# Kernel optimization log

Measured on AMD Instinct MI355X. Metric: run time of the kernel, lower is better.

Reference implementation:

```python
import jax, jax.numpy as jnp
import numpy as np

BS, SLEN, EM = 32, 4096, 256


def setup_inputs() -> dict:
    key = jax.random.key(0)
    ks = jax.random.split(key, 8)
    word_embedded = jax.random.normal(ks[0], (BS, SLEN, EM), dtype=jnp.float32)
    # valid-token mask: first `length` tokens valid per row (True = keep)
    lengths = jax.random.randint(ks[1], (BS, 1), SLEN // 2, SLEN + 1)
    mask = jnp.arange(SLEN)[None, :] < lengths  # (BS, SLEN) bool
    s = 1.0 / np.sqrt(EM)
    w_query = jax.random.uniform(ks[2], (EM, 1), minval=-1.0, maxval=1.0, dtype=jnp.float32)  # Linear(1, em, bias=False)
    wq = jax.random.uniform(ks[3], (EM, EM), minval=-s, maxval=s, dtype=jnp.float32)
    bq = jax.random.uniform(ks[4], (EM,), minval=-s, maxval=s, dtype=jnp.float32)
    wk = jax.random.uniform(ks[5], (EM, EM), minval=-s, maxval=s, dtype=jnp.float32)
    bk = jax.random.uniform(ks[6], (EM,), minval=-s, maxval=s, dtype=jnp.float32)
    se = 1.0 / np.sqrt(2 * EM)
    we = jax.random.uniform(ks[7], (1, 2 * EM), minval=-se, maxval=se, dtype=jnp.float32)
    be = jnp.zeros((1,), dtype=jnp.float32)
    return {"word_embedded": word_embedded, "mask": mask, "w_query": w_query,
            "wq": wq, "bq": bq, "wk": wk, "bk": bk, "we": we, "be": be}


def reference(word_embedded, mask, w_query, wq, bq, wk, bk, we, be):
    bs, slen, em = word_embedded.shape
    # query = Linear(1, em, no bias) applied to ones -> each row is w_query[:, 0]
    q = jnp.broadcast_to(w_query[:, 0], (bs, em))          # (bs, em)
    qp = jax.nn.relu(q @ wq.T + bq)                        # (bs, em); dropout is identity at eval
    k = jax.nn.relu(word_embedded @ wk.T + bk)             # (bs, slen, em)
    # proj_e(tanh(cat(q, k))) == tanh(q)@we_q + tanh(k)@we_k + be (tanh is elementwise),
    # so we avoid materializing the (bs, slen, 2*em) concat.
    we_q, we_k = we[0, :em], we[0, em:]
    energy = jnp.tanh(qp) @ we_q                           # (bs,)
    energy = energy[:, None] + jnp.tanh(k) @ we_k + be[0]  # (bs, slen)
    # torch: energy.masked_fill_(~mask, 1e-45)
    energy = jnp.where(mask, energy, jnp.float32(1e-45))
    attn_weights = jax.nn.softmax(energy, axis=1)          # (bs, slen)
    sent_embedded = jnp.einsum('bs,bse->be', attn_weights, word_embedded)  # (bs, em)
    return sent_embedded
```

## Files before the change

### kernel.cpp

```cpp
#include <hip/hip_runtime.h>

#define BS   32
#define SLEN 4096
#define EM   256
#define NROWS (BS * SLEN)

typedef __attribute__((ext_vector_type(8))) short bf16x8;
typedef __attribute__((ext_vector_type(4))) float f32x4;

#define WS_WKB   0
#define WS_EN    32768
#define WS_CONST 163840
#define WS_W     163856
#define WS_PART  294928

__device__ inline short f2bf(float x) {
  union { float f; unsigned u; } v; v.f = x;
  unsigned r = v.u + 0x7fffu + ((v.u >> 16) & 1u);
  return (short)(r >> 16);
}

#define GLOAD_LDS16(g, l)                                                  \
  __builtin_amdgcn_global_load_lds(                                        \
      (const __attribute__((address_space(1))) unsigned int*)(g),          \
      (__attribute__((address_space(3))) unsigned int*)(l), 16, 0, 0)

__global__ __launch_bounds__(256) void k0_cvt(const float* __restrict__ wk,
                                              unsigned short* __restrict__ wkb) {
  int idx = (blockIdx.x * 256 + threadIdx.x) * 4;
  float4 v = *(const float4*)(wk + idx);
  ushort4 o;
  o.x = (unsigned short)f2bf(v.x);
  o.y = (unsigned short)f2bf(v.y);
  o.z = (unsigned short)f2bf(v.z);
  o.w = (unsigned short)f2bf(v.w);
  *(ushort4*)(wkb + idx) = o;
}

__global__ __launch_bounds__(256) void k0b_qscalar(const float* __restrict__ w_query,
                                                   const float* __restrict__ wq,
                                                   const float* __restrict__ bq,
                                                   const float* __restrict__ we,
                                                   const float* __restrict__ be,
                                                   float* __restrict__ outc) {
  int t = threadIdx.x;
  float a = 0.f;
  const float* row = wq + (size_t)t * EM;
#pragma unroll 8
  for (int j = 0; j < EM; ++j) a = fmaf(row[j], w_query[j], a);
  a += bq[t];
  float v = we[t] * tanhf(fmaxf(a, 0.f));
#pragma unroll
  for (int off = 32; off >= 1; off >>= 1) v += __shfl_xor(v, off, 64);
  __shared__ float red[4];
  if ((t & 63) == 0) red[t >> 6] = v;
  __syncthreads();
  if (t == 0) outc[0] = red[0] + red[1] + red[2] + red[3] + be[0];
}

__global__ __launch_bounds__(256) void k1_energy(const float* __restrict__ X,
                                                 const unsigned short* __restrict__ wkb,
                                                 const float* __restrict__ bk,
                                                 const float* __restrict__ we,
                                                 float* __restrict__ energy) {
  __shared__ char lds[40960];
  char* As = lds;
  char* Bs = lds + 8192;
  const int tid = threadIdx.x;
  const int l = tid & 63;
  const int wid = tid >> 6;
  const int wr = wid >> 1, wc = wid & 1;
  const int row0 = blockIdx.x * 64;

  f32x4 acc[2][8];
#pragma unroll
  for (int i = 0; i < 2; ++i)
#pragma unroll
    for (int n = 0; n < 8; ++n) acc[i][n] = (f32x4){0.f, 0.f, 0.f, 0.f};

  const int egl = l >> 3;
  const int cg = (l & 7) ^ egl;

  for (int it = 0; it < 4; ++it) {
    const int k0 = it * 64;
#pragma unroll
    for (int q = 0; q < 8; ++q) {
      int seg = wid * 8 + q;
      int e = seg * 8 + egl;
      const char* g = (const char*)wkb + (size_t)e * 512 + k0 * 2 + cg * 16;
      GLOAD_LDS16(g, Bs + seg * 1024);
    }
#pragma unroll
    for (int p = 0; p < 2; ++p) {
      int n = tid + p * 256;
      int r = n >> 3, c = n & 7;
      const float* src = X + (size_t)(row0 + r) * EM + k0 + c * 8;
      float4 v0 = *(const float4*)(src);
      float4 v1 = *(const float4*)(src + 4);
      bf16x8 pk;
      pk[0] = f2bf(v0.x); pk[1] = f2bf(v0.y); pk[2] = f2bf(v0.z); pk[3] = f2bf(v0.w);
      pk[4] = f2bf(v1.x); pk[5] = f2bf(v1.y); pk[6] = f2bf(v1.z); pk[7] = f2bf(v1.w);
      *(bf16x8*)(As + r * 128 + ((c ^ (r & 7)) * 16)) = pk;
    }
    __syncthreads();
#pragma unroll
    for (int s = 0; s < 2; ++s) {
      const int swz0 = ((s * 4 + (l >> 4)) ^ (l & 7)) * 16;
      bf16x8 af[2], bfr[8];
#pragma unroll
      for (int i = 0; i < 2; ++i) {
        int row = wr * 32 + i * 16 + (l & 15);
        af[i] = *(const bf16x8*)(As + row * 128 + swz0);
      }
#pragma unroll
      for (int n = 0; n < 8; ++n) {
        int e = wc * 128 + n * 16 + (l & 15);
        bfr[n] = *(const bf16x8*)(Bs + e * 128 + swz0);
      }
#pragma unroll
      for (int i = 0; i < 2; ++i)
#pragma unroll
        for (int n = 0; n < 8; ++n)
          acc[i][n] = __builtin_amdgcn_mfma_f32_16x16x32_bf16(af[i], bfr[n], acc[i][n], 0, 0, 0);
    }
    __syncthreads();
  }

  float bkv[8], wev[8];
#pragma unroll
  for (int n = 0; n < 8; ++n) {
    int e = wc * 128 + n * 16 + (l & 15);
    bkv[n] = bk[e];
    wev[n] = we[EM + e];
  }
  float* ep = (float*)lds;
#pragma unroll
  for (int i = 0; i < 2; ++i) {
#pragma unroll
    for (int r = 0; r < 4; ++r) {
      float p = 0.f;
#pragma unroll
      for (int n = 0; n < 8; ++n) {
        float kv = fmaxf(acc[i][n][r] + bkv[n], 0.f);
        p += wev[n] * tanhf(kv);
      }
#pragma unroll
      for (int off = 1; off <= 8; off <<= 1) p += __shfl_xor(p, off, 64);
      if ((l & 15) == 0) {
        int row_local = wr * 32 + i * 16 + (l >> 4) * 4 + r;
        ep[row_local * 2 + wc] = p;
      }
    }
  }
  __syncthreads();
  if (tid < 64) energy[row0 + tid] = ep[tid * 2] + ep[tid * 2 + 1];
}

__global__ __launch_bounds__(256) void k2_softmax(const float* __restrict__ energy,
                                                  const unsigned char* __restrict__ mask,
                                                  const float* __restrict__ cptr,
                                                  float* __restrict__ wout) {
  const int b = blockIdx.x;
  const int t = threadIdx.x;
  const float C = cptr[0];
  const bool mask_is_byte = (mask[1] | mask[2] | mask[3]) != 0;
  const int* mask32 = (const int*)mask;
  const float* eb = energy + (size_t)b * SLEN;
  float v[16];
  float m = -3.4e38f;
#pragma unroll
  for (int i = 0; i < 16; ++i) {
    int s = t + i * 256;
    int mv = mask_is_byte ? (int)mask[(size_t)b * SLEN + s]
                          : mask32[(size_t)b * SLEN + s];
    float x = mv ? (eb[s] + C) : 1.4012984643248171e-45f;
    v[i] = x;
    m = fmaxf(m, x);
  }
  __shared__ float red[8];
#pragma unroll
  for (int off = 32; off >= 1; off >>= 1) m = fmaxf(m, __shfl_xor(m, off, 64));
  if ((t & 63) == 0) red[t >> 6] = m;
  __syncthreads();
  m = fmaxf(fmaxf(red[0], red[1]), fmaxf(red[2], red[3]));
  float s_ = 0.f;
#pragma unroll
  for (int i = 0; i < 16; ++i) {
    v[i] = expf(v[i] - m);
    s_ += v[i];
  }
#pragma unroll
  for (int off = 32; off >= 1; off >>= 1) s_ += __shfl_xor(s_, off, 64);
  if ((t & 63) == 0) red[4 + (t >> 6)] = s_;
  __syncthreads();
  float inv = 1.f / (red[4] + red[5] + red[6] + red[7]);
  float* wb = wout + (size_t)b * SLEN;
#pragma unroll
  for (int i = 0; i < 16; ++i) wb[t + i * 256] = v[i] * inv;
}

__global__ __launch_bounds__(256) void k3_wsum(const float* __restrict__ X,
                                               const float* __restrict__ w,
                                               float* __restrict__ part) {
  const int b = blockIdx.x >> 4;
  const int ch = blockIdx.x & 15;
  const int g = threadIdx.x >> 6;
  const int l = threadIdx.x & 63;
  const int s0 = ch * 256 + g * 64;
  const float* xb = X + (size_t)b * SLEN * EM;
  const float* wb = w + (size_t)b * SLEN;
  float4 acc = make_float4(0.f, 0.f, 0.f, 0.f);
#pragma unroll 4
  for (int i = 0; i < 64; ++i) {
    int s = s0 + i;
    float ws_ = wb[s];
    float4 v = *(const float4*)(xb + (size_t)s * EM + l * 4);
    acc.x = fmaf(ws_, v.x, acc.x);
    acc.y = fmaf(ws_, v.y, acc.y);
    acc.z = fmaf(ws_, v.z, acc.z);
    acc.w = fmaf(ws_, v.w, acc.w);
  }
  *(float4*)(part + ((size_t)((b * 16 + ch) * 4 + g)) * EM + l * 4) = acc;
}

__global__ __launch_bounds__(256) void k4_reduce(const float* __restrict__ part,
                                                 float* __restrict__ out) {
  const int b = blockIdx.x;
  const int e = threadIdx.x;
  float s = 0.f;
#pragma unroll 8
  for (int k = 0; k < 64; ++k) s += part[((size_t)b * 64 + k) * EM + e];
  out[(size_t)b * EM + e] = s;
}

extern "C" void kernel_launch(void* const* d_in, const int* in_sizes, int n_in,
                              void* d_out, int out_size, void* d_ws, size_t ws_size,
                              hipStream_t stream) {
  const float* X = (const float*)d_in[0];
  const unsigned char* mask = (const unsigned char*)d_in[1];
  const float* w_query = (const float*)d_in[2];
  const float* wq = (const float*)d_in[3];
  const float* bq = (const float*)d_in[4];
  const float* wk = (const float*)d_in[5];
  const float* bk = (const float*)d_in[6];
  const float* we = (const float*)d_in[7];
  const float* be = (const float*)d_in[8];
  float* out = (float*)d_out;
  float* ws = (float*)d_ws;

  unsigned short* wkb = (unsigned short*)(ws + WS_WKB);
  float* energy = ws + WS_EN;
  float* cscalar = ws + WS_CONST;
  float* weights = ws + WS_W;
  float* part = ws + WS_PART;

  k0_cvt<<<64, 256, 0, stream>>>(wk, wkb);
  k0b_qscalar<<<1, 256, 0, stream>>>(w_query, wq, bq, we, be, cscalar);
  k1_energy<<<NROWS / 64, 256, 0, stream>>>(X, wkb, bk, we, energy);
  k2_softmax<<<BS, 256, 0, stream>>>(energy, mask, cscalar, weights);
  k3_wsum<<<BS * 16, 256, 0, stream>>>(X, weights, part);
  k4_reduce<<<BS, 256, 0, stream>>>(part, out);
}
```

Before: 292.1 us.

## Load GEMM operands directly to registers, use fast tanh/exp, rebalance weighted-sum grid

The energy GEMM no longer stages X and Wk tiles through LDS with barriers. Each wave now loads its A fragments straight from global memory, converting to bf16 in registers, and reads B fragments directly from the bf16 weight buffer. tanhf and expf are replaced with fast exp-based approximations. The weighted-sum kernel uses twice as many blocks and reduces its four waves in LDS, which halves the partial buffer the final reduce reads. The trade-off is less data reuse across waves, since each wave re-reads Wk from cache, plus slightly lower accuracy from the approximate transcendentals.

```diff
diff --git a/kernel.cpp b/kernel.cpp
--- a/kernel.cpp
+++ b/kernel.cpp
@@ -20,10 +20,10 @@
   return (short)(r >> 16);
 }
 
-#define GLOAD_LDS16(g, l)                                                  \
-  __builtin_amdgcn_global_load_lds(                                        \
-      (const __attribute__((address_space(1))) unsigned int*)(g),          \
-      (__attribute__((address_space(3))) unsigned int*)(l), 16, 0, 0)
+__device__ inline float tanh_pos(float x) {
+  float e2 = __expf(2.f * x);
+  return 1.f - __fdividef(2.f, e2 + 1.f);
+}
 
 __global__ __launch_bounds__(256) void k0_cvt(const float* __restrict__ wk,
                                               unsigned short* __restrict__ wkb) {
@@ -49,7 +49,7 @@
 #pragma unroll 8
   for (int j = 0; j < EM; ++j) a = fmaf(row[j], w_query[j], a);
   a += bq[t];
-  float v = we[t] * tanhf(fmaxf(a, 0.f));
+  float v = we[t] * tanh_pos(fmaxf(a, 0.f));
 #pragma unroll
   for (int off = 32; off >= 1; off >>= 1) v += __shfl_xor(v, off, 64);
   __shared__ float red[4];
@@ -63,14 +63,15 @@
                                                  const float* __restrict__ bk,
                                                  const float* __restrict__ we,
                                                  float* __restrict__ energy) {
-  __shared__ char lds[40960];
-  char* As = lds;
-  char* Bs = lds + 8192;
+  __shared__ float ep[64][2];
   const int tid = threadIdx.x;
   const int l = tid & 63;
   const int wid = tid >> 6;
   const int wr = wid >> 1, wc = wid & 1;
+  const int lr = l & 15, lk = l >> 4;
   const int row0 = blockIdx.x * 64;
+  const float* xw = X + (size_t)(row0 + wr * 32 + lr) * EM;
+  const unsigned short* bw = wkb + (size_t)(wc * 128 + lr) * EM;
 
   f32x4 acc[2][8];
 #pragma unroll
@@ -78,62 +79,38 @@
 #pragma unroll
     for (int n = 0; n < 8; ++n) acc[i][n] = (f32x4){0.f, 0.f, 0.f, 0.f};
 
-  const int egl = l >> 3;
-  const int cg = (l & 7) ^ egl;
-
-  for (int it = 0; it < 4; ++it) {
-    const int k0 = it * 64;
-#pragma unroll
-    for (int q = 0; q < 8; ++q) {
-      int seg = wid * 8 + q;
-      int e = seg * 8 + egl;
-      const char* g = (const char*)wkb + (size_t)e * 512 + k0 * 2 + cg * 16;
-      GLOAD_LDS16(g, Bs + seg * 1024);
+#pragma unroll
+  for (int s = 0; s < 8; ++s) {
+    const int kf = s * 32 + lk * 8;
+    bf16x8 af[2];
+#pragma unroll
+    for (int i = 0; i < 2; ++i) {
+      const float* src = xw + (size_t)(i * 16) * EM + kf;
+      float4 v0 = *(const float4*)src;
+      float4 v1 = *(const float4*)(src + 4);
+      bf16x8 t;
+      t[0] = f2bf(v0.x); t[1] = f2bf(v0.y); t[2] = f2bf(v0.z); t[3] = f2bf(v0.w);
+      t[4] = f2bf(v1.x); t[5] = f2bf(v1.y); t[6] = f2bf(v1.z); t[7] = f2bf(v1.w);
+      af[i] = t;
     }
-#pragma unroll
-    for (int p = 0; p < 2; ++p) {
-      int n = tid + p * 256;
-      int r = n >> 3, c = n & 7;
-      const float* src = X + (size_t)(row0 + r) * EM + k0 + c * 8;
-      float4 v0 = *(const float4*)(src);
-      float4 v1 = *(const float4*)(src + 4);
-      bf16x8 pk;
-      pk[0] = f2bf(v0.x); pk[1] = f2bf(v0.y); pk[2] = f2bf(v0.z); pk[3] = f2bf(v0.w);
-      pk[4] = f2bf(v1.x); pk[5] = f2bf(v1.y); pk[6] = f2bf(v1.z); pk[7] = f2bf(v1.w);
-      *(bf16x8*)(As + r * 128 + ((c ^ (r & 7)) * 16)) = pk;
-    }
-    __syncthreads();
-#pragma unroll
-    for (int s = 0; s < 2; ++s) {
-      const int swz0 = ((s * 4 + (l >> 4)) ^ (l & 7)) * 16;
-      bf16x8 af[2], bfr[8];
-#pragma unroll
-      for (int i = 0; i < 2; ++i) {
-        int row = wr * 32 + i * 16 + (l & 15);
-        af[i] = *(const bf16x8*)(As + row * 128 + swz0);
-      }
-#pragma unroll
-      for (int n = 0; n < 8; ++n) {
-        int e = wc * 128 + n * 16 + (l & 15);
-        bfr[n] = *(const bf16x8*)(Bs + e * 128 + swz0);
-      }
-#pragma unroll
-      for (int i = 0; i < 2; ++i)
-#pragma unroll
-        for (int n = 0; n < 8; ++n)
-          acc[i][n] = __builtin_amdgcn_mfma_f32_16x16x32_bf16(af[i], bfr[n], acc[i][n], 0, 0, 0);
-    }
-    __syncthreads();
+    bf16x8 bfr[8];
+#pragma unroll
+    for (int n = 0; n < 8; ++n)
+      bfr[n] = *(const bf16x8*)(bw + (size_t)(n * 16) * EM + kf);
+#pragma unroll
+    for (int i = 0; i < 2; ++i)
+#pragma unroll
+      for (int n = 0; n < 8; ++n)
+        acc[i][n] = __builtin_amdgcn_mfma_f32_16x16x32_bf16(af[i], bfr[n], acc[i][n], 0, 0, 0);
   }
 
   float bkv[8], wev[8];
 #pragma unroll
   for (int n = 0; n < 8; ++n) {
-    int e = wc * 128 + n * 16 + (l & 15);
+    int e = wc * 128 + n * 16 + lr;
     bkv[n] = bk[e];
     wev[n] = we[EM + e];
   }
-  float* ep = (float*)lds;
 #pragma unroll
   for (int i = 0; i < 2; ++i) {
 #pragma unroll
@@ -142,18 +119,15 @@
 #pragma unroll
       for (int n = 0; n < 8; ++n) {
         float kv = fmaxf(acc[i][n][r] + bkv[n], 0.f);
-        p += wev[n] * tanhf(kv);
+        p += wev[n] * tanh_pos(kv);
       }
 #pragma unroll
       for (int off = 1; off <= 8; off <<= 1) p += __shfl_xor(p, off, 64);
-      if ((l & 15) == 0) {
-        int row_local = wr * 32 + i * 16 + (l >> 4) * 4 + r;
-        ep[row_local * 2 + wc] = p;
-      }
+      if (lr == 0) ep[wr * 32 + i * 16 + lk * 4 + r][wc] = p;
     }
   }
   __syncthreads();
-  if (tid < 64) energy[row0 + tid] = ep[tid * 2] + ep[tid * 2 + 1];
+  if (tid < 64) energy[row0 + tid] = ep[tid][0] + ep[tid][1];
 }
 
 __global__ __launch_bounds__(256) void k2_softmax(const float* __restrict__ energy,
@@ -186,7 +160,7 @@
   float s_ = 0.f;
 #pragma unroll
   for (int i = 0; i < 16; ++i) {
-    v[i] = expf(v[i] - m);
+    v[i] = __expf(v[i] - m);
     s_ += v[i];
   }
 #pragma unroll
@@ -202,16 +176,17 @@
 __global__ __launch_bounds__(256) void k3_wsum(const float* __restrict__ X,
                                                const float* __restrict__ w,
                                                float* __restrict__ part) {
-  const int b = blockIdx.x >> 4;
-  const int ch = blockIdx.x & 15;
+  __shared__ float red[4][EM];
+  const int b = blockIdx.x >> 5;
+  const int ch = blockIdx.x & 31;
   const int g = threadIdx.x >> 6;
   const int l = threadIdx.x & 63;
-  const int s0 = ch * 256 + g * 64;
+  const int s0 = ch * 128 + g * 32;
   const float* xb = X + (size_t)b * SLEN * EM;
   const float* wb = w + (size_t)b * SLEN;
   float4 acc = make_float4(0.f, 0.f, 0.f, 0.f);
 #pragma unroll 4
-  for (int i = 0; i < 64; ++i) {
+  for (int i = 0; i < 32; ++i) {
     int s = s0 + i;
     float ws_ = wb[s];
     float4 v = *(const float4*)(xb + (size_t)s * EM + l * 4);
@@ -220,7 +195,20 @@
     acc.z = fmaf(ws_, v.z, acc.z);
     acc.w = fmaf(ws_, v.w, acc.w);
   }
-  *(float4*)(part + ((size_t)((b * 16 + ch) * 4 + g)) * EM + l * 4) = acc;
+  *(float4*)(&red[g][l * 4]) = acc;
+  __syncthreads();
+  if (g == 0) {
+    float4 r0 = *(const float4*)(&red[0][l * 4]);
+    float4 r1 = *(const float4*)(&red[1][l * 4]);
+    float4 r2 = *(const float4*)(&red[2][l * 4]);
+    float4 r3 = *(const float4*)(&red[3][l * 4]);
+    float4 o;
+    o.x = (r0.x + r1.x) + (r2.x + r3.x);
+    o.y = (r0.y + r1.y) + (r2.y + r3.y);
+    o.z = (r0.z + r1.z) + (r2.z + r3.z);
+    o.w = (r0.w + r1.w) + (r2.w + r3.w);
+    *(float4*)(part + (size_t)(b * 32 + ch) * EM + l * 4) = o;
+  }
 }
 
 __global__ __launch_bounds__(256) void k4_reduce(const float* __restrict__ part,
@@ -229,7 +217,7 @@
   const int e = threadIdx.x;
   float s = 0.f;
 #pragma unroll 8
-  for (int k = 0; k < 64; ++k) s += part[((size_t)b * 64 + k) * EM + e];
+  for (int k = 0; k < 32; ++k) s += part[((size_t)b * 32 + k) * EM + e];
   out[(size_t)b * EM + e] = s;
 }
 
@@ -258,6 +246,6 @@
   k0b_qscalar<<<1, 256, 0, stream>>>(w_query, wq, bq, we, be, cscalar);
   k1_energy<<<NROWS / 64, 256, 0, stream>>>(X, wkb, bk, we, energy);
   k2_softmax<<<BS, 256, 0, stream>>>(energy, mask, cscalar, weights);
-  k3_wsum<<<BS * 16, 256, 0, stream>>>(X, weights, part);
+  k3_wsum<<<BS * 32, 256, 0, stream>>>(X, weights, part);
   k4_reduce<<<BS, 256, 0, stream>>>(part, out);
 }
```

Result: slower. 321.4 us (+10.0%).
